# Kernel tuning notes

Measured on AMD Instinct MI355X. Metric: run time of the kernel, lower is better.

## Reference

```python
import jax, jax.numpy as jnp
import numpy as np

D_MODEL = 1024
NHEAD = 16
HEAD_DIM = D_MODEL // NHEAD


def setup_inputs() -> dict:
    key = jax.random.key(0)
    ks = jax.random.split(key, 11)
    B, S = 2, 2048
    s = 1.0 / np.sqrt(D_MODEL)
    return {
        "query": jax.random.normal(ks[0], (B, S, D_MODEL), jnp.float32),
        "key": jax.random.normal(ks[1], (B, S, D_MODEL), jnp.float32),
        "value": jax.random.normal(ks[2], (B, S, D_MODEL), jnp.float32),
        "wq_w": jax.random.normal(ks[3], (D_MODEL, D_MODEL), jnp.float32) * s,
        "wq_b": jax.random.normal(ks[4], (D_MODEL,), jnp.float32) * s,
        "wk_w": jax.random.normal(ks[5], (D_MODEL, D_MODEL), jnp.float32) * s,
        "wk_b": jax.random.normal(ks[6], (D_MODEL,), jnp.float32) * s,
        "wv_w": jax.random.normal(ks[7], (D_MODEL, D_MODEL), jnp.float32) * s,
        "wv_b": jax.random.normal(ks[8], (D_MODEL,), jnp.float32) * s,
        "wo_w": jax.random.normal(ks[9], (D_MODEL, D_MODEL), jnp.float32) * s,
        "wo_b": jax.random.normal(ks[10], (D_MODEL,), jnp.float32) * s,
    }


def reference(query, key, value, wq_w, wq_b, wk_w, wk_b, wv_w, wv_b, wo_w, wo_b):
    B, S, _ = query.shape
    # torch Linear: x @ W.T + b
    def proj(x, w, b):
        y = x @ w.T + b
        return y.reshape(B, S, NHEAD, HEAD_DIM).transpose(0, 2, 1, 3)  # [B,H,S,Dh]

    Q = proj(query, wq_w, wq_b)
    K = proj(key, wk_w, wk_b)
    V = proj(value, wv_w, wv_b)

    scale = 1.0 / np.sqrt(HEAD_DIM).astype(np.float32)
    scores = jnp.einsum("bhqd,bhkd->bhqk", Q, K) * scale  # [B,H,S,S]
    causal = jnp.tril(jnp.ones((S, S), dtype=bool))
    scores = jnp.where(causal, scores, -jnp.inf)
    attn = jax.nn.softmax(scores, axis=-1)
    out = jnp.einsum("bhqk,bhkd->bhqd", attn, V)  # [B,H,S,Dh]
    out = out.transpose(0, 2, 1, 3).reshape(B, S, D_MODEL)
    return out @ wo_w.T + wo_b
```

## Files before the change

### kernel.cpp

```cpp
#include <hip/hip_runtime.h>
#include <stdint.h>

#define D_MODEL 1024
#define S_LEN   2048
#define NHEAD   16
#define HEAD_DIM 64
#define BATCH   2
#define M_TOT   (BATCH * S_LEN)
#define Q_SCALE 0.18033688011112042f

using bf16x8 = __attribute__((ext_vector_type(8))) short;
using f32x4  = __attribute__((ext_vector_type(4))) float;

__device__ __forceinline__ unsigned short f2bf(float f) {
  union { float f; unsigned int u; } v; v.f = f;
  unsigned int u = v.u;
  return (unsigned short)((u + 0x7FFFu + ((u >> 16) & 1u)) >> 16);
}
__device__ __forceinline__ unsigned int pkbf(float a, float b) {
#if __has_builtin(__builtin_amdgcn_cvt_pk_bf16_f32)
  auto p = __builtin_amdgcn_cvt_pk_bf16_f32(a, b);
  union { decltype(p) v; unsigned int u; } c; c.v = p;
  return c.u;
#else
  return (unsigned int)f2bf(a) | ((unsigned int)f2bf(b) << 16);
#endif
}
__device__ __forceinline__ bf16x8 cvt8(const float* p) {
  const float4 a = *(const float4*)p;
  const float4 b = *(const float4*)(p + 4);
  union { unsigned int u[4]; bf16x8 v; } r;
  r.u[0] = pkbf(a.x, a.y); r.u[1] = pkbf(a.z, a.w);
  r.u[2] = pkbf(b.x, b.y); r.u[3] = pkbf(b.z, b.w);
  return r.v;
}
__device__ __forceinline__ float fexp2(float x) {
#if __has_builtin(__builtin_amdgcn_exp2f)
  return __builtin_amdgcn_exp2f(x);
#else
  return __expf(x * 0.69314718055994531f);
#endif
}
__device__ __forceinline__ void async16(const unsigned short* g, short* l) {
  __builtin_amdgcn_global_load_lds(
      reinterpret_cast<const __attribute__((address_space(1))) unsigned int*>(
          reinterpret_cast<uintptr_t>(g)),
      reinterpret_cast<__attribute__((address_space(3))) unsigned int*>(
          reinterpret_cast<uintptr_t>(l)),
      16, 0, 0);
}

__device__ __forceinline__ void swap32(unsigned int& x, unsigned int& y) {
#if __has_builtin(__builtin_amdgcn_permlane32_swap)
  auto r = __builtin_amdgcn_permlane32_swap(x, y, false, false);
  x = (unsigned int)r[0]; y = (unsigned int)r[1];
#else
  const int lane = threadIdx.x & 63;
  unsigned int sx = (unsigned int)__shfl_xor((int)x, 32);
  unsigned int sy = (unsigned int)__shfl_xor((int)y, 32);
  unsigned int nx = (lane & 32) ? sy : x;
  unsigned int ny = (lane & 32) ? y : sx;
  x = nx; y = ny;
#endif
}
__device__ __forceinline__ void swap16(unsigned int& x, unsigned int& y) {
#if __has_builtin(__builtin_amdgcn_permlane16_swap)
  auto r = __builtin_amdgcn_permlane16_swap(x, y, false, false);
  x = (unsigned int)r[0]; y = (unsigned int)r[1];
#else
  const int lane = threadIdx.x & 63;
  unsigned int sx = (unsigned int)__shfl_xor((int)x, 16);
  unsigned int sy = (unsigned int)__shfl_xor((int)y, 16);
  unsigned int nx = (lane & 16) ? sy : x;
  unsigned int ny = (lane & 16) ? y : sx;
  x = nx; y = ny;
#endif
}

#define LDK 40

__global__ __launch_bounds__(256)
void cast_all(const float* __restrict__ wq, const float* __restrict__ wk,
              const float* __restrict__ wv, const float* __restrict__ wo,
              const float* __restrict__ q, const float* __restrict__ k,
              const float* __restrict__ v,
              unsigned short* __restrict__ wb,
              unsigned short* __restrict__ qb, unsigned short* __restrict__ kb,
              unsigned short* __restrict__ vb)
{
  const int z = blockIdx.y;
  const float* src;
  unsigned short* d;
  size_t n;
  switch (z) {
    case 0: src = wq; d = wb;                                   n = (size_t)D_MODEL * D_MODEL; break;
    case 1: src = wk; d = wb + (size_t)1 * D_MODEL * D_MODEL;   n = (size_t)D_MODEL * D_MODEL; break;
    case 2: src = wv; d = wb + (size_t)2 * D_MODEL * D_MODEL;   n = (size_t)D_MODEL * D_MODEL; break;
    case 3: src = wo; d = wb + (size_t)3 * D_MODEL * D_MODEL;   n = (size_t)D_MODEL * D_MODEL; break;
    case 4: src = q;  d = qb;                                   n = (size_t)M_TOT * D_MODEL;   break;
    case 5: src = k;  d = kb;                                   n = (size_t)M_TOT * D_MODEL;   break;
    default: src = v; d = vb;                                   n = (size_t)M_TOT * D_MODEL;   break;
  }
  const size_t i = ((size_t)blockIdx.x * 256 + threadIdx.x) * 8;
  if (i < n) *(bf16x8*)(d + i) = cvt8(src + i);
}

__device__ __forceinline__ void gemm_tile_lds(const unsigned short* __restrict__ A,
                                              const unsigned short* __restrict__ W,
                                              int m0, int n0,
                                              short* As, short* Bs,
                                              f32x4 acc[4][4])
{
  const int t    = threadIdx.x;
  const int lane = t & 63;
  const int w    = t >> 6;
  const int quad = lane >> 4;
  const int l16  = lane & 15;
  const int wm   = (w >> 1) * 64;
  const int wn   = (w & 1) * 64;
  const int srow = w * 16 + (lane >> 2);
  const int scol = (lane & 3) * 8;

  for (int mt = 0; mt < 4; ++mt)
    for (int nt = 0; nt < 4; ++nt)
      acc[mt][nt] = f32x4{0.f, 0.f, 0.f, 0.f};

  for (int kt = 0; kt < D_MODEL / 32; ++kt) {
    const int kc = kt * 32 + scol;
    __syncthreads();
    async16(A + (size_t)(m0 + srow)      * D_MODEL + kc, As + srow * 32 + scol);
    async16(A + (size_t)(m0 + 64 + srow) * D_MODEL + kc, As + (64 + srow) * 32 + scol);
    async16(W + (size_t)(n0 + srow)      * D_MODEL + kc, Bs + srow * 32 + scol);
    async16(W + (size_t)(n0 + 64 + srow) * D_MODEL + kc, Bs + (64 + srow) * 32 + scol);
    __syncthreads();

    bf16x8 af[4], bfr[4];
    for (int mt = 0; mt < 4; ++mt)
      af[mt] = *(const bf16x8*)(As + (wm + mt * 16 + l16) * 32 + quad * 8);
    for (int nt = 0; nt < 4; ++nt)
      bfr[nt] = *(const bf16x8*)(Bs + (wn + nt * 16 + l16) * 32 + quad * 8);
    for (int mt = 0; mt < 4; ++mt)
      for (int nt = 0; nt < 4; ++nt)
        acc[mt][nt] = __builtin_amdgcn_mfma_f32_16x16x32_bf16(af[mt], bfr[nt], acc[mt][nt], 0, 0, 0);
  }
}

__device__ __forceinline__ void gemm_tile_f32(const float* __restrict__ A,
                                              const unsigned short* __restrict__ W,
                                              int m0, int n0,
                                              short* As, short* Bs,
                                              f32x4 acc[4][4])
{
  const int t    = threadIdx.x;
  const int lane = t & 63;
  const int w    = t >> 6;
  const int quad = lane >> 4;
  const int l16  = lane & 15;
  const int wm   = (w >> 1) * 64;
  const int wn   = (w & 1) * 64;
  const int srow = t >> 2;
  const int scol = (t & 3) * 8;

  for (int mt = 0; mt < 4; ++mt)
    for (int nt = 0; nt < 4; ++nt)
      acc[mt][nt] = f32x4{0.f, 0.f, 0.f, 0.f};

  for (int kt = 0; kt < D_MODEL / 32; ++kt) {
    const int kc = kt * 32 + scol;
    const bf16x8 a0 = cvt8(A + (size_t)(m0 + srow)      * D_MODEL + kc);
    const bf16x8 a1 = cvt8(A + (size_t)(m0 + srow + 64) * D_MODEL + kc);
    const bf16x8 b0 = *(const bf16x8*)(W + (size_t)(n0 + srow)      * D_MODEL + kc);
    const bf16x8 b1 = *(const bf16x8*)(W + (size_t)(n0 + srow + 64) * D_MODEL + kc);
    __syncthreads();
    *(bf16x8*)(As + (srow)      * LDK + scol) = a0;
    *(bf16x8*)(As + (srow + 64) * LDK + scol) = a1;
    *(bf16x8*)(Bs + (srow)      * LDK + scol) = b0;
    *(bf16x8*)(Bs + (srow + 64) * LDK + scol) = b1;
    __syncthreads();

    bf16x8 af[4], bfr[4];
    for (int mt = 0; mt < 4; ++mt)
      af[mt] = *(const bf16x8*)(As + (wm + mt * 16 + l16) * LDK + quad * 8);
    for (int nt = 0; nt < 4; ++nt)
      bfr[nt] = *(const bf16x8*)(Bs + (wn + nt * 16 + l16) * LDK + quad * 8);
    for (int mt = 0; mt < 4; ++mt)
      for (int nt = 0; nt < 4; ++nt)
        acc[mt][nt] = __builtin_amdgcn_mfma_f32_16x16x32_bf16(af[mt], bfr[nt], acc[mt][nt], 0, 0, 0);
  }
}

__device__ __forceinline__ void qkv_epilogue(int z, int m0, int n0,
                                             const float* __restrict__ bias,
                                             float scale,
                                             unsigned short* __restrict__ dst,
                                             f32x4 acc[4][4])
{
  const int t    = threadIdx.x;
  const int lane = t & 63;
  const int w    = t >> 6;
  const int quad = lane >> 4;
  const int l16  = lane & 15;
  const int wm   = (w >> 1) * 64;
  const int wn   = (w & 1) * 64;

  for (int nt = 0; nt < 4; ++nt) {
    const int n = n0 + wn + nt * 16 + l16;
    const float bb = bias[n];
    const int h = n >> 6, d = n & 63;
    for (int mt = 0; mt < 4; ++mt) {
      for (int r = 0; r < 4; ++r) {
        const int m = m0 + wm + mt * 16 + quad * 4 + r;
        const int b = m >> 11, s = m & 2047;
        const unsigned short val = f2bf((acc[mt][nt][r] + bb) * scale);
        if (z < 2)
          dst[((size_t)((b * NHEAD + h) * S_LEN + s)) * HEAD_DIM + d] = val;
        else
          dst[((size_t)((b * NHEAD + h) * HEAD_DIM + d)) * S_LEN + s] = val;
      }
    }
  }
}

__global__ __launch_bounds__(256)
void qkv_fast(const unsigned short* __restrict__ qb,
              const unsigned short* __restrict__ kb,
              const unsigned short* __restrict__ vb,
              const unsigned short* __restrict__ wqb,
              const unsigned short* __restrict__ wkb,
              const unsigned short* __restrict__ wvb,
              const float* __restrict__ bq, const float* __restrict__ bk,
              const float* __restrict__ bv,
              unsigned short* __restrict__ Qh, unsigned short* __restrict__ Kh,
              unsigned short* __restrict__ VhT)
{
  __shared__ __attribute__((aligned(16))) short As[128 * 32];
  __shared__ __attribute__((aligned(16))) short Bs[128 * 32];
  const int z = blockIdx.z;
  const unsigned short* A    = (z == 0) ? qb  : (z == 1) ? kb  : vb;
  const unsigned short* W    = (z == 0) ? wqb : (z == 1) ? wkb : wvb;
  const float*          bias = (z == 0) ? bq  : (z == 1) ? bk  : bv;
  unsigned short*       dst  = (z == 0) ? Qh  : (z == 1) ? Kh  : VhT;
  const float           scale = (z == 0) ? Q_SCALE : 1.0f;

  const int m0 = blockIdx.x * 128, n0 = blockIdx.y * 128;
  f32x4 acc[4][4];
  gemm_tile_lds(A, W, m0, n0, As, Bs, acc);
  qkv_epilogue(z, m0, n0, bias, scale, dst, acc);
}

__global__ __launch_bounds__(256)
void qkv_slow(const float* __restrict__ query, const float* __restrict__ key,
              const float* __restrict__ value,
              const unsigned short* __restrict__ wqb,
              const unsigned short* __restrict__ wkb,
              const unsigned short* __restrict__ wvb,
              const float* __restrict__ bq, const float* __restrict__ bk,
              const float* __restrict__ bv,
              unsigned short* __restrict__ Qh, unsigned short* __restrict__ Kh,
              unsigned short* __restrict__ VhT)
{
  __shared__ __attribute__((aligned(16))) short As[128 * LDK];
  __shared__ __attribute__((aligned(16))) short Bs[128 * LDK];
  const int z = blockIdx.z;
  const float*          A    = (z == 0) ? query : (z == 1) ? key : value;
  const unsigned short* W    = (z == 0) ? wqb   : (z == 1) ? wkb : wvb;
  const float*          bias = (z == 0) ? bq    : (z == 1) ? bk  : bv;
  unsigned short*       dst  = (z == 0) ? Qh    : (z == 1) ? Kh  : VhT;
  const float           scale = (z == 0) ? Q_SCALE : 1.0f;

  const int m0 = blockIdx.x * 128, n0 = blockIdx.y * 128;
  f32x4 acc[4][4];
  gemm_tile_f32(A, W, m0, n0, As, Bs, acc);
  qkv_epilogue(z, m0, n0, bias, scale, dst, acc);
}

__global__ __launch_bounds__(256)
void out_proj(const unsigned short* __restrict__ Oh,
              const unsigned short* __restrict__ wob,
              const float* __restrict__ bo,
              float* __restrict__ dst)
{
  __shared__ __attribute__((aligned(16))) short As[128 * 32];
  __shared__ __attribute__((aligned(16))) short Bs[128 * 32];
  const int m0 = blockIdx.x * 128, n0 = blockIdx.y * 128;
  f32x4 acc[4][4];
  gemm_tile_lds(Oh, wob, m0, n0, As, Bs, acc);

  const int t    = threadIdx.x;
  const int lane = t & 63;
  const int w    = t >> 6;
  const int quad = lane >> 4;
  const int l16  = lane & 15;
  const int wm   = (w >> 1) * 64;
  const int wn   = (w & 1) * 64;

  for (int nt = 0; nt < 4; ++nt) {
    const int n = n0 + wn + nt * 16 + l16;
    const float bb = bo[n];
    for (int mt = 0; mt < 4; ++mt)
      for (int r = 0; r < 4; ++r) {
        const int m = m0 + wm + mt * 16 + quad * 4 + r;
        dst[(size_t)m * D_MODEL + n] = acc[mt][nt][r] + bb;
      }
  }
}

struct Frags { bf16x8 ka0, ka1, kb0, kb1, v0, v1, v2, v3; };
struct StageRegs { bf16x8 k0, k1, k2, k3, v0, v1, v2, v3; };

#define KS_LD 72
#define VT_LD 136

__device__ __forceinline__ StageRegs load_stage(const unsigned short* __restrict__ Kb,
                                                const unsigned short* __restrict__ Vb,
                                                int k0, int kr, int kc, int vd, int vc) {
  StageRegs r;
  r.k0 = *(const bf16x8*)(Kb + (size_t)(k0 + kr)      * HEAD_DIM + kc);
  r.k1 = *(const bf16x8*)(Kb + (size_t)(k0 + kr + 32) * HEAD_DIM + kc);
  r.k2 = *(const bf16x8*)(Kb + (size_t)(k0 + kr + 64) * HEAD_DIM + kc);
  r.k3 = *(const bf16x8*)(Kb + (size_t)(k0 + kr + 96) * HEAD_DIM + kc);
  r.v0 = *(const bf16x8*)(Vb + (size_t)(vd)      * S_LEN + k0 + vc);
  r.v1 = *(const bf16x8*)(Vb + (size_t)(vd + 16) * S_LEN + k0 + vc);
  r.v2 = *(const bf16x8*)(Vb + (size_t)(vd + 32) * S_LEN + k0 + vc);
  r.v3 = *(const bf16x8*)(Vb + (size_t)(vd + 48) * S_LEN + k0 + vc);
  return r;
}
__device__ __forceinline__ void write_stage(const StageRegs& r, short* Ks, short* Vts,
                                            int kr, int kc, int vd, int vc) {
  *(bf16x8*)(Ks + (kr)      * KS_LD + kc) = r.k0;
  *(bf16x8*)(Ks + (kr + 32) * KS_LD + kc) = r.k1;
  *(bf16x8*)(Ks + (kr + 64) * KS_LD + kc) = r.k2;
  *(bf16x8*)(Ks + (kr + 96) * KS_LD + kc) = r.k3;
  *(bf16x8*)(Vts + (vd)      * VT_LD + vc) = r.v0;
  *(bf16x8*)(Vts + (vd + 16) * VT_LD + vc) = r.v1;
  *(bf16x8*)(Vts + (vd + 32) * VT_LD + vc) = r.v2;
  *(bf16x8*)(Vts + (vd + 48) * VT_LD + vc) = r.v3;
}
__device__ __forceinline__ Frags lds_frags(const short* Ks, const short* Vts,
                                           int c, int quad, int l16) {
  Frags f;
  const short* kp = Ks + (c * 32 + l16) * KS_LD + quad * 8;
  f.ka0 = *(const bf16x8*)(kp);
  f.ka1 = *(const bf16x8*)(kp + 32);
  f.kb0 = *(const bf16x8*)(kp + 16 * KS_LD);
  f.kb1 = *(const bf16x8*)(kp + 16 * KS_LD + 32);
  const short* vp = Vts + l16 * VT_LD + c * 32 + quad * 8;
  f.v0 = *(const bf16x8*)(vp);
  f.v1 = *(const bf16x8*)(vp + 16 * VT_LD);
  f.v2 = *(const bf16x8*)(vp + 32 * VT_LD);
  f.v3 = *(const bf16x8*)(vp + 48 * VT_LD);
  return f;
}

template <bool DIAG>
__device__ __forceinline__ void proc_chunk(const Frags& f, const bf16x8 qf[2][2],
                                           const bf16x8& ones, int quad, int l16,
                                           f32x4 lacc[2], f32x4 oacc[2][4]) {
  f32x4 sA0 = f32x4{0.f, 0.f, 0.f, 0.f};
  f32x4 sA1 = f32x4{0.f, 0.f, 0.f, 0.f};
  f32x4 sB0 = f32x4{0.f, 0.f, 0.f, 0.f};
  f32x4 sB1 = f32x4{0.f, 0.f, 0.f, 0.f};
  sA0 = __builtin_amdgcn_mfma_f32_16x16x32_bf16(f.ka0, qf[0][0], sA0, 0, 0, 0);
  sA0 = __builtin_amdgcn_mfma_f32_16x16x32_bf16(f.ka1, qf[0][1], sA0, 0, 0, 0);
  sA1 = __builtin_amdgcn_mfma_f32_16x16x32_bf16(f.ka0, qf[1][0], sA1, 0, 0, 0);
  sA1 = __builtin_amdgcn_mfma_f32_16x16x32_bf16(f.ka1, qf[1][1], sA1, 0, 0, 0);
  if (!DIAG) {
    sB0 = __builtin_amdgcn_mfma_f32_16x16x32_bf16(f.kb0, qf[0][0], sB0, 0, 0, 0);
    sB0 = __builtin_amdgcn_mfma_f32_16x16x32_bf16(f.kb1, qf[0][1], sB0, 0, 0, 0);
  }
  sB1 = __builtin_amdgcn_mfma_f32_16x16x32_bf16(f.kb0, qf[1][0], sB1, 0, 0, 0);
  sB1 = __builtin_amdgcn_mfma_f32_16x16x32_bf16(f.kb1, qf[1][1], sB1, 0, 0, 0);

  float stA0[4], stB0[4], stA1[4], stB1[4];
  const int kl = quad * 4;
#pragma unroll
  for (int r = 0; r < 4; ++r) {
    if (!DIAG) {
      stA0[r] = fexp2(sA0[r]);
      stB0[r] = fexp2(sB0[r]);
      stB1[r] = fexp2(sB1[r]);
    } else {
      stA0[r] = (kl + r <= l16) ? fexp2(sA0[r]) : 0.f;
      stB0[r] = 0.f;
      stB1[r] = (kl + r <= l16) ? fexp2(sB1[r]) : 0.f;
    }
    stA1[r] = fexp2(sA1[r]);
  }

  unsigned int a0 = pkbf(stA0[0], stA0[1]), b0 = pkbf(stA0[2], stA0[3]);
  unsigned int c0_ = pkbf(stB0[0], stB0[1]), e0 = pkbf(stB0[2], stB0[3]);
  swap32(a0, c0_); swap32(b0, e0);
  swap16(a0, c0_); swap16(b0, e0);
  union { unsigned int u[4]; bf16x8 v; } p0;
  p0.u[0] = a0; p0.u[1] = b0; p0.u[2] = c0_; p0.u[3] = e0;
  unsigned int a1 = pkbf(stA1[0], stA1[1]), b1 = pkbf(stA1[2], stA1[3]);
  unsigned int c1_ = pkbf(stB1[0], stB1[1]), e1 = pkbf(stB1[2], stB1[3]);
  swap32(a1, c1_); swap32(b1, e1);
  swap16(a1, c1_); swap16(b1, e1);
  union { unsigned int u[4]; bf16x8 v; } p1;
  p1.u[0] = a1; p1.u[1] = b1; p1.u[2] = c1_; p1.u[3] = e1;

  lacc[0] = __builtin_amdgcn_mfma_f32_16x16x32_bf16(p0.v, ones, lacc[0], 0, 0, 0);
  lacc[1] = __builtin_amdgcn_mfma_f32_16x16x32_bf16(p1.v, ones, lacc[1], 0, 0, 0);
  oacc[0][0] = __builtin_amdgcn_mfma_f32_16x16x32_bf16(p0.v, f.v0, oacc[0][0], 0, 0, 0);
  oacc[1][0] = __builtin_amdgcn_mfma_f32_16x16x32_bf16(p1.v, f.v0, oacc[1][0], 0, 0, 0);
  oacc[0][1] = __builtin_amdgcn_mfma_f32_16x16x32_bf16(p0.v, f.v1, oacc[0][1], 0, 0, 0);
  oacc[1][1] = __builtin_amdgcn_mfma_f32_16x16x32_bf16(p1.v, f.v1, oacc[1][1], 0, 0, 0);
  oacc[0][2] = __builtin_amdgcn_mfma_f32_16x16x32_bf16(p0.v, f.v2, oacc[0][2], 0, 0, 0);
  oacc[1][2] = __builtin_amdgcn_mfma_f32_16x16x32_bf16(p1.v, f.v2, oacc[1][2], 0, 0, 0);
  oacc[0][3] = __builtin_amdgcn_mfma_f32_16x16x32_bf16(p0.v, f.v3, oacc[0][3], 0, 0, 0);
  oacc[1][3] = __builtin_amdgcn_mfma_f32_16x16x32_bf16(p1.v, f.v3, oacc[1][3], 0, 0, 0);
}

__global__ __launch_bounds__(256)
void attn_kernel(const unsigned short* __restrict__ Qh,
                 const unsigned short* __restrict__ Kh,
                 const unsigned short* __restrict__ VhT,
                 unsigned short* __restrict__ O)
{
  __shared__ __attribute__((aligned(16))) short Ks[128 * KS_LD];
  __shared__ __attribute__((aligned(16))) short Vts[64 * VT_LD];

  const int orig = blockIdx.x;
  const int xcd  = orig & 7;
  const int li   = orig >> 3;
  const int bh   = xcd * 4 + (li & 3);
  const int qt   = 15 - (li >> 2);
  const int q0   = qt * 128;
  const int b    = bh >> 4;
  const int h    = bh & 15;
  const int t    = threadIdx.x;
  const int w    = t >> 6;
  const int lane = t & 63;
  const int quad = lane >> 4;
  const int l16  = lane & 15;
  const int rowbase = q0 + w * 32;

  const unsigned short* Kb = Kh + (size_t)bh * S_LEN * HEAD_DIM;
  const unsigned short* Vb = VhT + (size_t)bh * HEAD_DIM * S_LEN;
  const int kr = t >> 3, kc = (t & 7) * 8;
  const int vd = t >> 4, vc = (t & 15) * 8;

  bf16x8 qf[2][2];
#pragma unroll
  for (int mt = 0; mt < 2; ++mt) {
    const size_t qrow = (size_t)bh * S_LEN + rowbase + mt * 16 + l16;
    qf[mt][0] = *(const bf16x8*)(Qh + qrow * HEAD_DIM + quad * 8);
    qf[mt][1] = *(const bf16x8*)(Qh + qrow * HEAD_DIM + 32 + quad * 8);
  }
  bf16x8 ones;
#pragma unroll
  for (int j = 0; j < 8; ++j) ones[j] = (short)0x3F80;

  f32x4 lacc[2];
  f32x4 oacc[2][4];
  lacc[0] = f32x4{0.f, 0.f, 0.f, 0.f};
  lacc[1] = f32x4{0.f, 0.f, 0.f, 0.f};
#pragma unroll
  for (int mt = 0; mt < 2; ++mt)
#pragma unroll
    for (int dt = 0; dt < 4; ++dt) oacc[mt][dt] = f32x4{0.f, 0.f, 0.f, 0.f};

  const int nT = qt + 1;
  StageRegs rs = load_stage(Kb, Vb, 0, kr, kc, vd, vc);
  for (int j = 0; j < nT; ++j) {
    __syncthreads();
    write_stage(rs, Ks, Vts, kr, kc, vd, vc);
    __syncthreads();
    if (j + 1 < nT) rs = load_stage(Kb, Vb, (j + 1) * 128, kr, kc, vd, vc);
    if (j < qt) {
#pragma unroll
      for (int c = 0; c < 4; ++c) {
        const Frags f = lds_frags(Ks, Vts, c, quad, l16);
        proc_chunk<false>(f, qf, ones, quad, l16, lacc, oacc);
      }
    } else {
      for (int c = 0; c < w; ++c) {
        const Frags f = lds_frags(Ks, Vts, c, quad, l16);
        proc_chunk<false>(f, qf, ones, quad, l16, lacc, oacc);
      }
      const Frags f = lds_frags(Ks, Vts, w, quad, l16);
      proc_chunk<true>(f, qf, ones, quad, l16, lacc, oacc);
    }
  }

#pragma unroll
  for (int mt = 0; mt < 2; ++mt)
#pragma unroll
    for (int dt = 0; dt < 4; ++dt)
#pragma unroll
      for (int r = 0; r < 4; ++r) {
        const int rowg = rowbase + mt * 16 + quad * 4 + r;
        O[(size_t)(b * S_LEN + rowg) * D_MODEL + h * 64 + dt * 16 + l16] =
            f2bf(oacc[mt][dt][r] / lacc[mt][r]);
      }
}

extern "C" void kernel_launch(void* const* d_in, const int* in_sizes, int n_in,
                              void* d_out, int out_size, void* d_ws, size_t ws_size,
                              hipStream_t stream)
{
  (void)in_sizes; (void)n_in; (void)out_size;
  const float* q  = (const float*)d_in[0];
  const float* k  = (const float*)d_in[1];
  const float* v  = (const float*)d_in[2];
  const float* wq = (const float*)d_in[3];
  const float* bq = (const float*)d_in[4];
  const float* wk = (const float*)d_in[5];
  const float* bk = (const float*)d_in[6];
  const float* wv = (const float*)d_in[7];
  const float* bv = (const float*)d_in[8];
  const float* wo = (const float*)d_in[9];
  const float* bo = (const float*)d_in[10];
  float* out = (float*)d_out;

  unsigned short* wb  = (unsigned short*)d_ws;
  unsigned short* wqb = wb;
  unsigned short* wkb = wb + (size_t)1 * D_MODEL * D_MODEL;
  unsigned short* wvb = wb + (size_t)2 * D_MODEL * D_MODEL;
  unsigned short* wob = wb + (size_t)3 * D_MODEL * D_MODEL;
  unsigned short* Kh  = wb + (size_t)4 * D_MODEL * D_MODEL;
  unsigned short* VhT = Kh + (size_t)M_TOT * D_MODEL;
  unsigned short* Oh  = VhT + (size_t)M_TOT * D_MODEL;
  unsigned short* qb  = Oh;
  unsigned short* vb  = Oh + (size_t)M_TOT * D_MODEL;
  unsigned short* Qh  = (unsigned short*)d_out;
  unsigned short* kb  = Qh + (size_t)M_TOT * D_MODEL;

  const bool fast = ws_size >= (size_t)40 * 1024 * 1024;

  dim3 g1(M_TOT / 128, D_MODEL / 128, 3);
  if (fast) {
    dim3 gc((size_t)M_TOT * D_MODEL / (256 * 8), 7, 1);
    cast_all<<<gc, 256, 0, stream>>>(wq, wk, wv, wo, q, k, v, wb, qb, kb, vb);
    qkv_fast<<<g1, 256, 0, stream>>>(qb, kb, vb, wqb, wkb, wvb, bq, bk, bv, Qh, Kh, VhT);
  } else {
    dim3 gc((size_t)D_MODEL * D_MODEL / (256 * 8), 4, 1);
    cast_all<<<gc, 256, 0, stream>>>(wq, wk, wv, wo, q, k, v, wb, qb, kb, vb);
    qkv_slow<<<g1, 256, 0, stream>>>(q, k, v, wqb, wkb, wvb, bq, bk, bv, Qh, Kh, VhT);
  }

  dim3 g2(512, 1, 1);
  attn_kernel<<<g2, 256, 0, stream>>>(Qh, Kh, VhT, Oh);

  dim3 g3(M_TOT / 128, D_MODEL / 128, 1);
  out_proj<<<g3, 256, 0, stream>>>(Oh, wob, bo, out);
}
```

Baseline: 217.1 us.

## Double-buffer K/V LDS tiles in attention, add MFMA priority hints, vectorize V store

After: 226.5 us. 1.04x slower.

```diff
diff --git a/kernel.cpp b/kernel.cpp
--- a/kernel.cpp
+++ b/kernel.cpp
@@ -11,6 +11,7 @@
 
 using bf16x8 = __attribute__((ext_vector_type(8))) short;
 using f32x4  = __attribute__((ext_vector_type(4))) float;
+using u16x4  = __attribute__((ext_vector_type(4))) unsigned short;
 
 __device__ __forceinline__ unsigned short f2bf(float f) {
   union { float f; unsigned int u; } v; v.f = f;
@@ -203,19 +204,34 @@
   const int wm   = (w >> 1) * 64;
   const int wn   = (w & 1) * 64;
 
-  for (int nt = 0; nt < 4; ++nt) {
-    const int n = n0 + wn + nt * 16 + l16;
-    const float bb = bias[n];
-    const int h = n >> 6, d = n & 63;
-    for (int mt = 0; mt < 4; ++mt) {
-      for (int r = 0; r < 4; ++r) {
-        const int m = m0 + wm + mt * 16 + quad * 4 + r;
+  if (z < 2) {
+    for (int nt = 0; nt < 4; ++nt) {
+      const int n = n0 + wn + nt * 16 + l16;
+      const float bb = bias[n];
+      const int h = n >> 6, d = n & 63;
+      for (int mt = 0; mt < 4; ++mt) {
+        for (int r = 0; r < 4; ++r) {
+          const int m = m0 + wm + mt * 16 + quad * 4 + r;
+          const int b = m >> 11, s = m & 2047;
+          dst[((size_t)((b * NHEAD + h) * S_LEN + s)) * HEAD_DIM + d] =
+              f2bf((acc[mt][nt][r] + bb) * scale);
+        }
+      }
+    }
+  } else {
+    for (int nt = 0; nt < 4; ++nt) {
+      const int n = n0 + wn + nt * 16 + l16;
+      const float bb = bias[n];
+      const int h = n >> 6, d = n & 63;
+      for (int mt = 0; mt < 4; ++mt) {
+        const int m = m0 + wm + mt * 16 + quad * 4;
         const int b = m >> 11, s = m & 2047;
-        const unsigned short val = f2bf((acc[mt][nt][r] + bb) * scale);
-        if (z < 2)
-          dst[((size_t)((b * NHEAD + h) * S_LEN + s)) * HEAD_DIM + d] = val;
-        else
-          dst[((size_t)((b * NHEAD + h) * HEAD_DIM + d)) * S_LEN + s] = val;
+        u16x4 pk;
+        pk[0] = f2bf(acc[mt][nt][0] + bb);
+        pk[1] = f2bf(acc[mt][nt][1] + bb);
+        pk[2] = f2bf(acc[mt][nt][2] + bb);
+        pk[3] = f2bf(acc[mt][nt][3] + bb);
+        *(u16x4*)(dst + ((size_t)((b * NHEAD + h) * HEAD_DIM + d)) * S_LEN + s) = pk;
       }
     }
   }
@@ -360,6 +376,7 @@
   f32x4 sA1 = f32x4{0.f, 0.f, 0.f, 0.f};
   f32x4 sB0 = f32x4{0.f, 0.f, 0.f, 0.f};
   f32x4 sB1 = f32x4{0.f, 0.f, 0.f, 0.f};
+  __builtin_amdgcn_s_setprio(1);
   sA0 = __builtin_amdgcn_mfma_f32_16x16x32_bf16(f.ka0, qf[0][0], sA0, 0, 0, 0);
   sA0 = __builtin_amdgcn_mfma_f32_16x16x32_bf16(f.ka1, qf[0][1], sA0, 0, 0, 0);
   sA1 = __builtin_amdgcn_mfma_f32_16x16x32_bf16(f.ka0, qf[1][0], sA1, 0, 0, 0);
@@ -370,6 +387,7 @@
   }
   sB1 = __builtin_amdgcn_mfma_f32_16x16x32_bf16(f.kb0, qf[1][0], sB1, 0, 0, 0);
   sB1 = __builtin_amdgcn_mfma_f32_16x16x32_bf16(f.kb1, qf[1][1], sB1, 0, 0, 0);
+  __builtin_amdgcn_s_setprio(0);
 
   float stA0[4], stB0[4], stA1[4], stB1[4];
   const int kl = quad * 4;
@@ -400,6 +418,7 @@
   union { unsigned int u[4]; bf16x8 v; } p1;
   p1.u[0] = a1; p1.u[1] = b1; p1.u[2] = c1_; p1.u[3] = e1;
 
+  __builtin_amdgcn_s_setprio(1);
   lacc[0] = __builtin_amdgcn_mfma_f32_16x16x32_bf16(p0.v, ones, lacc[0], 0, 0, 0);
   lacc[1] = __builtin_amdgcn_mfma_f32_16x16x32_bf16(p1.v, ones, lacc[1], 0, 0, 0);
   oacc[0][0] = __builtin_amdgcn_mfma_f32_16x16x32_bf16(p0.v, f.v0, oacc[0][0], 0, 0, 0);
@@ -410,6 +429,7 @@
   oacc[1][2] = __builtin_amdgcn_mfma_f32_16x16x32_bf16(p1.v, f.v2, oacc[1][2], 0, 0, 0);
   oacc[0][3] = __builtin_amdgcn_mfma_f32_16x16x32_bf16(p0.v, f.v3, oacc[0][3], 0, 0, 0);
   oacc[1][3] = __builtin_amdgcn_mfma_f32_16x16x32_bf16(p1.v, f.v3, oacc[1][3], 0, 0, 0);
+  __builtin_amdgcn_s_setprio(0);
 }
 
 __global__ __launch_bounds__(256)
@@ -418,8 +438,8 @@
                  const unsigned short* __restrict__ VhT,
                  unsigned short* __restrict__ O)
 {
-  __shared__ __attribute__((aligned(16))) short Ks[128 * KS_LD];
-  __shared__ __attribute__((aligned(16))) short Vts[64 * VT_LD];
+  __shared__ __attribute__((aligned(16))) short Ks[2][128 * KS_LD];
+  __shared__ __attribute__((aligned(16))) short Vts[2][64 * VT_LD];
 
   const int orig = blockIdx.x;
   const int xcd  = orig & 7;
@@ -463,25 +483,31 @@
 
   const int nT = qt + 1;
   StageRegs rs = load_stage(Kb, Vb, 0, kr, kc, vd, vc);
+  write_stage(rs, Ks[0], Vts[0], kr, kc, vd, vc);
+  __syncthreads();
   for (int j = 0; j < nT; ++j) {
-    __syncthreads();
-    write_stage(rs, Ks, Vts, kr, kc, vd, vc);
-    __syncthreads();
-    if (j + 1 < nT) rs = load_stage(Kb, Vb, (j + 1) * 128, kr, kc, vd, vc);
+    const short* Ksj = (j & 1) ? Ks[1] : Ks[0];
+    const short* Vtj = (j & 1) ? Vts[1] : Vts[0];
+    short* Ksn = (j & 1) ? Ks[0] : Ks[1];
+    short* Vtn = (j & 1) ? Vts[0] : Vts[1];
+    const bool more = (j + 1 < nT);
+    if (more) rs = load_stage(Kb, Vb, (j + 1) * 128, kr, kc, vd, vc);
     if (j < qt) {
 #pragma unroll
       for (int c = 0; c < 4; ++c) {
-        const Frags f = lds_frags(Ks, Vts, c, quad, l16);
+        const Frags f = lds_frags(Ksj, Vtj, c, quad, l16);
         proc_chunk<false>(f, qf, ones, quad, l16, lacc, oacc);
       }
     } else {
       for (int c = 0; c < w; ++c) {
-        const Frags f = lds_frags(Ks, Vts, c, quad, l16);
+        const Frags f = lds_frags(Ksj, Vtj, c, quad, l16);
         proc_chunk<false>(f, qf, ones, quad, l16, lacc, oacc);
       }
-      const Frags f = lds_frags(Ks, Vts, w, quad, l16);
+      const Frags f = lds_frags(Ksj, Vtj, w, quad, l16);
       proc_chunk<true>(f, qf, ones, quad, l16, lacc, oacc);
     }
+    if (more) write_stage(rs, Ksn, Vtn, kr, kc, vd, vc);
+    __syncthreads();
   }
 
 #pragma unroll
```
